# Kernel tuning notes

Measured on AMD Instinct MI355X. Metric: run time of the kernel, lower is better.

## Reference

```python
import jax, jax.numpy as jnp
import numpy as np
from jax import lax

# init_kwargs constants
DO_TUBE = False
TAU = 0.3
ITERATIONS = 5
BLEND_FACTOR = 0.3


def _avg_pool3(x):
    """3x3x3 avg pool, stride 1, zero padding 1, count_include_pad=True.
    x: (n, h, w, d). Matches torch F.avg_pool3d(kernel=3, stride=1, padding=1)."""
    s = lax.reduce_window(x, 0.0, lax.add, (1, 3, 3, 3), (1, 1, 1, 1), 'SAME')
    return s * (1.0 / 27.0)


def setup_inputs() -> dict:
    key = jax.random.key(0)
    # binary mask (b, 1, h, w, d) as docstring requires
    u = jax.random.uniform(key, (2, 1, 256, 256, 256), dtype=jnp.float32)
    seg = (u > 0.5).astype(jnp.float32)
    return {"segmentation": seg}


def reference(segmentation):
    b, c, h, w, d = segmentation.shape
    x = segmentation.reshape(b * c, h, w, d)

    # NOTE: in the original code `mask` is never updated inside the iteration
    # loop, so every iteration adds the identical term; the loop over the
    # batch dim is also trivially batchable. Compute the per-iteration term
    # once (fully batched) and scale by ITERATIONS.
    eroded = -_avg_pool3(-x)            # differentiable erosion
    dilated = _avg_pool3(eroded)        # differentiable dilation
    diff = x - dilated
    term = jax.nn.sigmoid((diff - 0.5) / TAU) + diff  # soft_threshold + residual
    skeleton = ITERATIONS * term

    skeleton = skeleton.reshape(b, c, h, w, d)
    # DO_TUBE is False (the torch code path for True is broken for 5D input)
    skeleton = BLEND_FACTOR * segmentation + (1.0 - BLEND_FACTOR) * skeleton
    skeleton = jnp.round(jnp.clip(skeleton, 0.0, 1.0))
    return 1.0 - skeleton
```

## Files before the change

### kernel.cpp

```cpp
#include <hip/hip_runtime.h>
#include <stdint.h>


typedef float  vfloat4 __attribute__((ext_vector_type(4)));

#define CH 8
#define NCHUNK 32
#define BLOCKS 4096

__device__ __forceinline__ uint32_t row_pack(uint32_t b, const int ln) {
    uint32_t up = (uint32_t)__builtin_amdgcn_update_dpp(
        0, (int)b, 0x138, 0xf, 0xf, true);
    uint32_t dn = (uint32_t)__builtin_amdgcn_update_dpp(
        0, (int)b, 0x130, 0xf, 0xf, true);
    uint64_t W = (uint64_t)(up >> 16) | ((uint64_t)b << 16)
               | ((uint64_t)(dn & 0xffffu) << 48);
    uint64_t S = W + ((W >> 8) << 1) + (W >> 16) * 3u + ((W >> 24) << 1) + (W >> 32);
    uint32_t n = (uint32_t)S;
    if (ln == 0)  n -= (b & 0xffu);
    if (ln == 63) n -= (b & 0xff000000u);
    return n | (b << 7);
}

__device__ __forceinline__ uint32_t bits_of(const vfloat4 v) {
    return (v.x > 0.5f ? 0x1u : 0u) | (v.y > 0.5f ? 0x100u : 0u)
         | (v.z > 0.5f ? 0x10000u : 0u) | (v.w > 0.5f ? 0x1000000u : 0u);
}

__global__ __launch_bounds__(256) void skel_k1(const float* __restrict__ x,
                                               uint32_t* __restrict__ ws) {
    const int ln    = threadIdx.x & 63;
    const int wid   = (blockIdx.x << 2) | (threadIdx.x >> 6);
    const int chunk = wid & (NCHUNK - 1);
    const int slab  = wid >> 5;
    const int w0    = chunk * CH;
    const vfloat4* xs = (const vfloat4*)(x + (size_t)slab * 65536);
    uint32_t* os = ws + (size_t)slab * 16384;

    auto ldraw = [&](int wi) -> vfloat4 {
        int wc = wi < 0 ? 0 : (wi > 255 ? 255 : wi);
        return xs[wc * 64 + ln];
    };
    auto packb = [&](vfloat4 v, int wi) -> uint32_t {
        uint32_t b = bits_of(v);
        return (wi >= 0 && wi < 256) ? b : 0u;
    };

    vfloat4 a0 = ldraw(w0 - 2), a1 = ldraw(w0 - 1), a2 = ldraw(w0),
            a3 = ldraw(w0 + 1), a4 = ldraw(w0 + 2);
    vfloat4 raw0 = ldraw(w0 + 3), raw1 = ldraw(w0 + 4),
            raw2 = ldraw(w0 + 5), raw3 = ldraw(w0 + 6);
    uint32_t r0 = row_pack(packb(a0, w0 - 2), ln);
    uint32_t r1 = row_pack(packb(a1, w0 - 1), ln);
    uint32_t r2 = row_pack(packb(a2, w0    ), ln);
    uint32_t r3 = row_pack(packb(a3, w0 + 1), ln);
    uint32_t r4 = row_pack(packb(a4, w0 + 2), ln);

    for (int g = 0; g < CH; g += 4) {
        vfloat4 n0 = ldraw(w0 + g + 7),  n1 = ldraw(w0 + g + 8),
                n2 = ldraw(w0 + g + 9),  n3 = ldraw(w0 + g + 10);
        vfloat4 cur[4] = {raw0, raw1, raw2, raw3};
        #pragma unroll
        for (int j = 0; j < 4; ++j) {
            const int w = w0 + g + j;
            uint32_t rn = row_pack(packb(cur[j], w + 3), ln);
            uint32_t m0 = r0 & 0x7f7f7f7fu, m1 = r1 & 0x7f7f7f7fu,
                     m2 = r2 & 0x7f7f7f7fu, m3 = r3 & 0x7f7f7f7fu,
                     m4 = r4 & 0x7f7f7f7fu;
            uint32_t s = m0 + (m1 << 1) + m2 * 3u + (m3 << 1) + m4;
            if (w == 0 || w == 255) s -= m2;
            s |= (r2 & 0x80808080u);
            os[w * 64 + ln] = s;
            r0 = r1; r1 = r2; r2 = r3; r3 = r4; r4 = rn;
        }
        raw0 = n0; raw1 = n1; raw2 = n2; raw3 = n3;
    }
}

__global__ __launch_bounds__(256) void skel_k2(const uint32_t* __restrict__ ws,
                                               vfloat4* __restrict__ out) {
    const int ln    = threadIdx.x & 63;
    const int wid   = (blockIdx.x << 2) | (threadIdx.x >> 6);
    const int chunk = wid & (NCHUNK - 1);
    const int col   = wid >> 5;
    const int wi    = col & 255, bi = col >> 8;
    const int h0    = chunk * CH;
    const uint32_t base = (uint32_t)bi * (1u << 22) + (uint32_t)wi * 64u + (uint32_t)ln;

    auto ld = [&](int hi) -> uint32_t {
        int hc = hi < 0 ? 0 : (hi > 255 ? 255 : hi);
        return ws[base + (uint32_t)hc * 16384u];
    };
    auto msk = [&](uint32_t q, int hi) -> uint32_t {
        return (hi >= 0 && hi < 256) ? q : 0u;
    };

    uint32_t q0 = msk(ld(h0 - 2), h0 - 2), q1 = msk(ld(h0 - 1), h0 - 1),
             q2 = ld(h0), q3 = ld(h0 + 1), q4 = ld(h0 + 2);
    uint32_t p0 = ld(h0 + 3), p1 = ld(h0 + 4), p2 = ld(h0 + 5), p3 = ld(h0 + 6);

    for (int g = 0; g < CH; g += 4) {
        uint32_t f0 = ld(h0 + g + 7),  f1 = ld(h0 + g + 8),
                 f2 = ld(h0 + g + 9),  f3 = ld(h0 + g + 10);
        uint32_t cur[4] = {p0, p1, p2, p3};
        #pragma unroll
        for (int j = 0; j < 4; ++j) {
            const int h = h0 + g + j;
            uint32_t qn = msk(cur[j], h + 3);
            uint32_t m0 = q0 & 0x7f7f7f7fu, m1 = q1 & 0x7f7f7f7fu,
                     m2 = q2 & 0x7f7f7f7fu, m3 = q3 & 0x7f7f7f7fu,
                     m4 = q4 & 0x7f7f7f7fu;
            uint32_t e0 = m0 & 0x00ff00ffu, e1 = m1 & 0x00ff00ffu,
                     e2 = m2 & 0x00ff00ffu, e3 = m3 & 0x00ff00ffu,
                     e4 = m4 & 0x00ff00ffu;
            uint32_t o0 = (m0 >> 8) & 0x00ff00ffu, o1 = (m1 >> 8) & 0x00ff00ffu,
                     o2 = (m2 >> 8) & 0x00ff00ffu, o3 = (m3 >> 8) & 0x00ff00ffu,
                     o4 = (m4 >> 8) & 0x00ff00ffu;
            uint32_t ae = e0 + (e1 << 1) + e2 * 3u + (e3 << 1) + e4;
            uint32_t ao = o0 + (o1 << 1) + o2 * 3u + (o3 << 1) + o4;
            if (h == 0 || h == 255) { ae -= e2; ao -= o2; }
            const uint32_t xb = q2;
            vfloat4 o;
            o.x = ((ae & 0xffffu) >= 9u && !((xb >> 7)  & 1u)) ? 1.0f : 0.0f;
            o.y = ((ao & 0xffffu) >= 9u && !((xb >> 15) & 1u)) ? 1.0f : 0.0f;
            o.z = ((ae >> 16)     >= 9u && !((xb >> 23) & 1u)) ? 1.0f : 0.0f;
            o.w = ((ao >> 16)     >= 9u && !((xb >> 31) & 1u)) ? 1.0f : 0.0f;
            __builtin_nontemporal_store(o, &out[base + (uint32_t)h * 16384u]);
            q0 = q1; q1 = q2; q2 = q3; q3 = q4; q4 = qn;
        }
        p0 = f0; p1 = f1; p2 = f2; p3 = f3;
    }
}

extern "C" void kernel_launch(void* const* d_in, const int* in_sizes, int n_in,
                              void* d_out, int out_size, void* d_ws, size_t ws_size,
                              hipStream_t stream) {
    const float* x = (const float*)d_in[0];
    uint32_t* ws = (uint32_t*)d_ws;
    skel_k1<<<BLOCKS, 256, 0, stream>>>(x, ws);
    skel_k2<<<BLOCKS, 256, 0, stream>>>(ws, (vfloat4*)d_out);
}
```

Measured before the change: 235.0 us.

## Restructure H-pass to per-row W-sweep and interleave two slabs in W-pass

The first kernel now has each wavefront handle two slabs at once, each with a 16-row W chunk, which halves the halo reload overhead per output and gives more independent loads in flight. The second kernel no longer streams along H with a sliding window. Each wavefront now takes one H row and sweeps 16 W positions, loading five H-neighbour rows each step and prefetching the next step, so output stores become contiguous along W. This trades the register-carried reuse along H for 5x reads of the workspace, which should mostly hit cache, in exchange for better store locality and fewer halo loads. Grid sizes change to match.

```diff
diff --git a/kernel.cpp b/kernel.cpp
--- a/kernel.cpp
+++ b/kernel.cpp
@@ -4,9 +4,13 @@
 
 typedef float  vfloat4 __attribute__((ext_vector_type(4)));
 
-#define CH 8
-#define NCHUNK 32
-#define BLOCKS 4096
+#define CH1 16
+#define NCH1 16
+#define BLOCKS_K1 1024
+
+#define CW2 16
+#define NCW2 16
+#define BLOCKS_K2 2048
 
 __device__ __forceinline__ uint32_t row_pack(uint32_t b, const int ln) {
     uint32_t up = (uint32_t)__builtin_amdgcn_update_dpp(
@@ -31,49 +35,71 @@
                                                uint32_t* __restrict__ ws) {
     const int ln    = threadIdx.x & 63;
     const int wid   = (blockIdx.x << 2) | (threadIdx.x >> 6);
-    const int chunk = wid & (NCHUNK - 1);
-    const int slab  = wid >> 5;
-    const int w0    = chunk * CH;
-    const vfloat4* xs = (const vfloat4*)(x + (size_t)slab * 65536);
-    uint32_t* os = ws + (size_t)slab * 16384;
+    const int chunk = wid & (NCH1 - 1);
+    const int sp    = wid >> 4;
+    const int w0    = chunk * CH1;
 
-    auto ldraw = [&](int wi) -> vfloat4 {
+    const vfloat4* xs[2] = {
+        (const vfloat4*)(x + (size_t)(2 * sp)     * 65536),
+        (const vfloat4*)(x + (size_t)(2 * sp + 1) * 65536)};
+    uint32_t* os[2] = { ws + (size_t)(2 * sp)     * 16384,
+                        ws + (size_t)(2 * sp + 1) * 16384 };
+
+    auto ldx = [&](int c, int wi) -> vfloat4 {
         int wc = wi < 0 ? 0 : (wi > 255 ? 255 : wi);
-        return xs[wc * 64 + ln];
+        return xs[c][wc * 64 + ln];
     };
     auto packb = [&](vfloat4 v, int wi) -> uint32_t {
         uint32_t b = bits_of(v);
         return (wi >= 0 && wi < 256) ? b : 0u;
     };
 
-    vfloat4 a0 = ldraw(w0 - 2), a1 = ldraw(w0 - 1), a2 = ldraw(w0),
-            a3 = ldraw(w0 + 1), a4 = ldraw(w0 + 2);
-    vfloat4 raw0 = ldraw(w0 + 3), raw1 = ldraw(w0 + 4),
-            raw2 = ldraw(w0 + 5), raw3 = ldraw(w0 + 6);
-    uint32_t r0 = row_pack(packb(a0, w0 - 2), ln);
-    uint32_t r1 = row_pack(packb(a1, w0 - 1), ln);
-    uint32_t r2 = row_pack(packb(a2, w0    ), ln);
-    uint32_t r3 = row_pack(packb(a3, w0 + 1), ln);
-    uint32_t r4 = row_pack(packb(a4, w0 + 2), ln);
+    uint32_t r[2][5];
+    vfloat4  raw[2][4];
+    #pragma unroll
+    for (int c = 0; c < 2; ++c) {
+        vfloat4 a[5];
+        #pragma unroll
+        for (int i = 0; i < 5; ++i) a[i] = ldx(c, w0 - 2 + i);
+        #pragma unroll
+        for (int t = 0; t < 4; ++t) raw[c][t] = ldx(c, w0 + 3 + t);
+        #pragma unroll
+        for (int i = 0; i < 5; ++i)
+            r[c][i] = row_pack(packb(a[i], w0 - 2 + i), ln);
+    }
 
-    for (int g = 0; g < CH; g += 4) {
-        vfloat4 n0 = ldraw(w0 + g + 7),  n1 = ldraw(w0 + g + 8),
-                n2 = ldraw(w0 + g + 9),  n3 = ldraw(w0 + g + 10);
-        vfloat4 cur[4] = {raw0, raw1, raw2, raw3};
+    #pragma unroll
+    for (int g = 0; g < CH1; g += 4) {
+        vfloat4 n[2][4];
+        if (g + 4 < CH1) {
+            #pragma unroll
+            for (int c = 0; c < 2; ++c)
+                #pragma unroll
+                for (int t = 0; t < 4; ++t) n[c][t] = ldx(c, w0 + g + 7 + t);
+        }
         #pragma unroll
-        for (int j = 0; j < 4; ++j) {
-            const int w = w0 + g + j;
-            uint32_t rn = row_pack(packb(cur[j], w + 3), ln);
-            uint32_t m0 = r0 & 0x7f7f7f7fu, m1 = r1 & 0x7f7f7f7fu,
-                     m2 = r2 & 0x7f7f7f7fu, m3 = r3 & 0x7f7f7f7fu,
-                     m4 = r4 & 0x7f7f7f7fu;
-            uint32_t s = m0 + (m1 << 1) + m2 * 3u + (m3 << 1) + m4;
-            if (w == 0 || w == 255) s -= m2;
-            s |= (r2 & 0x80808080u);
-            os[w * 64 + ln] = s;
-            r0 = r1; r1 = r2; r2 = r3; r3 = r4; r4 = rn;
+        for (int c = 0; c < 2; ++c) {
+            #pragma unroll
+            for (int j = 0; j < 4; ++j) {
+                const int w = w0 + g + j;
+                uint32_t rn = row_pack(packb(raw[c][j], w + 3), ln);
+                uint32_t m0 = r[c][0] & 0x7f7f7f7fu, m1 = r[c][1] & 0x7f7f7f7fu,
+                         m2 = r[c][2] & 0x7f7f7f7fu, m3 = r[c][3] & 0x7f7f7f7fu,
+                         m4 = r[c][4] & 0x7f7f7f7fu;
+                uint32_t s = m0 + (m1 << 1) + m2 * 3u + (m3 << 1) + m4;
+                if (w == 0 || w == 255) s -= m2;
+                s |= (r[c][2] & 0x80808080u);
+                os[c][w * 64 + ln] = s;
+                r[c][0] = r[c][1]; r[c][1] = r[c][2];
+                r[c][2] = r[c][3]; r[c][3] = r[c][4]; r[c][4] = rn;
+            }
         }
-        raw0 = n0; raw1 = n1; raw2 = n2; raw3 = n3;
+        if (g + 4 < CH1) {
+            #pragma unroll
+            for (int c = 0; c < 2; ++c)
+                #pragma unroll
+                for (int t = 0; t < 4; ++t) raw[c][t] = n[c][t];
+        }
     }
 }
 
@@ -81,54 +107,57 @@
                                                vfloat4* __restrict__ out) {
     const int ln    = threadIdx.x & 63;
     const int wid   = (blockIdx.x << 2) | (threadIdx.x >> 6);
-    const int chunk = wid & (NCHUNK - 1);
-    const int col   = wid >> 5;
-    const int wi    = col & 255, bi = col >> 8;
-    const int h0    = chunk * CH;
-    const uint32_t base = (uint32_t)bi * (1u << 22) + (uint32_t)wi * 64u + (uint32_t)ln;
+    const int chunk = wid & (NCW2 - 1);
+    const int slab  = wid >> 4;
+    const int hi    = slab & 255, bi = slab >> 8;
+    const int w0    = chunk * CW2;
 
-    auto ld = [&](int hi) -> uint32_t {
-        int hc = hi < 0 ? 0 : (hi > 255 ? 255 : hi);
-        return ws[base + (uint32_t)hc * 16384u];
-    };
-    auto msk = [&](uint32_t q, int hi) -> uint32_t {
-        return (hi >= 0 && hi < 256) ? q : 0u;
-    };
+    uint32_t rowbase[5];
+    uint32_t rmask[5];
+    #pragma unroll
+    for (int k = 0; k < 5; ++k) {
+        const int hk = hi - 2 + k;
+        const int hc = hk < 0 ? 0 : (hk > 255 ? 255 : hk);
+        rowbase[k] = ((uint32_t)bi * 256u + (uint32_t)hc) * 16384u
+                   + (uint32_t)w0 * 64u + (uint32_t)ln;
+        rmask[k]   = (hk >= 0 && hk <= 255) ? 0x7f7f7f7fu : 0u;
+    }
+    const bool hbound = (hi == 0 || hi == 255);
+    const uint32_t obase = (uint32_t)slab * 16384u + (uint32_t)w0 * 64u
+                         + (uint32_t)ln;
 
-    uint32_t q0 = msk(ld(h0 - 2), h0 - 2), q1 = msk(ld(h0 - 1), h0 - 1),
-             q2 = ld(h0), q3 = ld(h0 + 1), q4 = ld(h0 + 2);
-    uint32_t p0 = ld(h0 + 3), p1 = ld(h0 + 4), p2 = ld(h0 + 5), p3 = ld(h0 + 6);
+    uint32_t cur[5], nxt[5];
+    #pragma unroll
+    for (int k = 0; k < 5; ++k) { cur[k] = ws[rowbase[k]]; nxt[k] = cur[k]; }
 
-    for (int g = 0; g < CH; g += 4) {
-        uint32_t f0 = ld(h0 + g + 7),  f1 = ld(h0 + g + 8),
-                 f2 = ld(h0 + g + 9),  f3 = ld(h0 + g + 10);
-        uint32_t cur[4] = {p0, p1, p2, p3};
+    #pragma unroll
+    for (int j = 0; j < CW2; ++j) {
+        if (j + 1 < CW2) {
+            #pragma unroll
+            for (int k = 0; k < 5; ++k)
+                nxt[k] = ws[rowbase[k] + (uint32_t)(j + 1) * 64u];
+        }
+        const uint32_t m0 = cur[0] & rmask[0], m1 = cur[1] & rmask[1],
+                       m2 = cur[2] & rmask[2], m3 = cur[3] & rmask[3],
+                       m4 = cur[4] & rmask[4];
+        const uint32_t e0 = m0 & 0x00ff00ffu, e1 = m1 & 0x00ff00ffu,
+                       e2 = m2 & 0x00ff00ffu, e3 = m3 & 0x00ff00ffu,
+                       e4 = m4 & 0x00ff00ffu;
+        const uint32_t o0 = (m0 >> 8) & 0x00ff00ffu, o1 = (m1 >> 8) & 0x00ff00ffu,
+                       o2 = (m2 >> 8) & 0x00ff00ffu, o3 = (m3 >> 8) & 0x00ff00ffu,
+                       o4 = (m4 >> 8) & 0x00ff00ffu;
+        uint32_t ae = e0 + (e1 << 1) + e2 * 3u + (e3 << 1) + e4;
+        uint32_t ao = o0 + (o1 << 1) + o2 * 3u + (o3 << 1) + o4;
+        if (hbound) { ae -= e2; ao -= o2; }
+        const uint32_t xb = cur[2];
+        vfloat4 o;
+        o.x = ((ae & 0xffffu) >= 9u && !((xb >> 7)  & 1u)) ? 1.0f : 0.0f;
+        o.y = ((ao & 0xffffu) >= 9u && !((xb >> 15) & 1u)) ? 1.0f : 0.0f;
+        o.z = ((ae >> 16)     >= 9u && !((xb >> 23) & 1u)) ? 1.0f : 0.0f;
+        o.w = ((ao >> 16)     >= 9u && !((xb >> 31) & 1u)) ? 1.0f : 0.0f;
+        __builtin_nontemporal_store(o, &out[obase + (uint32_t)j * 64u]);
         #pragma unroll
-        for (int j = 0; j < 4; ++j) {
-            const int h = h0 + g + j;
-            uint32_t qn = msk(cur[j], h + 3);
-            uint32_t m0 = q0 & 0x7f7f7f7fu, m1 = q1 & 0x7f7f7f7fu,
-                     m2 = q2 & 0x7f7f7f7fu, m3 = q3 & 0x7f7f7f7fu,
-                     m4 = q4 & 0x7f7f7f7fu;
-            uint32_t e0 = m0 & 0x00ff00ffu, e1 = m1 & 0x00ff00ffu,
-                     e2 = m2 & 0x00ff00ffu, e3 = m3 & 0x00ff00ffu,
-                     e4 = m4 & 0x00ff00ffu;
-            uint32_t o0 = (m0 >> 8) & 0x00ff00ffu, o1 = (m1 >> 8) & 0x00ff00ffu,
-                     o2 = (m2 >> 8) & 0x00ff00ffu, o3 = (m3 >> 8) & 0x00ff00ffu,
-                     o4 = (m4 >> 8) & 0x00ff00ffu;
-            uint32_t ae = e0 + (e1 << 1) + e2 * 3u + (e3 << 1) + e4;
-            uint32_t ao = o0 + (o1 << 1) + o2 * 3u + (o3 << 1) + o4;
-            if (h == 0 || h == 255) { ae -= e2; ao -= o2; }
-            const uint32_t xb = q2;
-            vfloat4 o;
-            o.x = ((ae & 0xffffu) >= 9u && !((xb >> 7)  & 1u)) ? 1.0f : 0.0f;
-            o.y = ((ao & 0xffffu) >= 9u && !((xb >> 15) & 1u)) ? 1.0f : 0.0f;
-            o.z = ((ae >> 16)     >= 9u && !((xb >> 23) & 1u)) ? 1.0f : 0.0f;
-            o.w = ((ao >> 16)     >= 9u && !((xb >> 31) & 1u)) ? 1.0f : 0.0f;
-            __builtin_nontemporal_store(o, &out[base + (uint32_t)h * 16384u]);
-            q0 = q1; q1 = q2; q2 = q3; q3 = q4; q4 = qn;
-        }
-        p0 = f0; p1 = f1; p2 = f2; p3 = f3;
+        for (int k = 0; k < 5; ++k) cur[k] = nxt[k];
     }
 }
 
@@ -137,6 +166,6 @@
                               hipStream_t stream) {
     const float* x = (const float*)d_in[0];
     uint32_t* ws = (uint32_t*)d_ws;
-    skel_k1<<<BLOCKS, 256, 0, stream>>>(x, ws);
-    skel_k2<<<BLOCKS, 256, 0, stream>>>(ws, (vfloat4*)d_out);
+    skel_k1<<<BLOCKS_K1, 256, 0, stream>>>(x, ws);
+    skel_k2<<<BLOCKS_K2, 256, 0, stream>>>(ws, (vfloat4*)d_out);
 }
```

After: 249.3 us. 1.06x slower.
